# Performance work log

Measured on AMD Instinct MI355X. Metric: run time of the kernel, lower is better.

The kernel has to match this reference:

```python
import jax, jax.numpy as jnp
import numpy as np

N_SEQ, L, DH, DX, M, G, N_TOK, N_MEM, N_TYP = 1024, 64, 256, 128, 8192, 4096, 10000, 262144, 64

def setup_inputs() -> dict:
    key = jax.random.key(0)
    ks = jax.random.split(key, 16)
    s_q = 1.0 / np.sqrt(2 * DH)
    s_k = 1.0 / np.sqrt(DH)
    s_r = 1.0 / np.sqrt(2 * DH + DX)
    msk = jax.random.randint(ks[4], (N_SEQ, L), 0, 2).astype(jnp.int32)
    msk = msk.at[:, 0].set(1)  # guarantee >=1 valid position per sequence
    return {
        "mem": jax.random.randint(ks[0], (N_MEM,), 0, N_TOK),
        "grp": jax.random.randint(ks[1], (N_MEM,), 0, G),
        "pos2grp": jax.random.randint(ks[2], (N_SEQ, L), 0, G),
        "h_grp": jax.random.normal(ks[3], (N_SEQ, L, DH), jnp.float32),
        "msk": msk,
        "idx": jnp.sort(jax.random.randint(ks[5], (M,), 0, N_SEQ)),
        "src": jax.random.randint(ks[6], (M,), 0, L),
        "dst": jax.random.randint(ks[7], (M,), 0, L),
        "typ": jax.random.randint(ks[8], (M, N_TYP), 0, 2).astype(jnp.int32),
        "tok_emb": jax.random.normal(ks[9], (N_TOK, DX), jnp.float32),
        "Wq": jax.random.normal(ks[10], (2 * DH, DH), jnp.float32) * s_q,
        "bq": jnp.zeros((DH,), jnp.float32),
        "Wk": jax.random.normal(ks[11], (DH, DH), jnp.float32) * s_k,
        "bk": jnp.zeros((DH,), jnp.float32),
        "Wrel": jax.random.normal(ks[12], (2 * DH + DX, N_TYP), jnp.float32) * s_r,
        "brel": jnp.zeros((N_TYP,), jnp.float32),
    }

def reference(mem, grp, pos2grp, h_grp, msk, idx, src, dst, typ,
              tok_emb, Wq, bq, Wk, bk, Wrel, brel):
    # z_grp = scatter_sum(tok_encoder(mem), grp, 0)[pos2grp]  -> (n, l, dx)
    z = jax.ops.segment_sum(tok_emb[mem], grp, num_segments=G)
    z_grp = z[pos2grp]
    # q = cat(h_grp[idx, src], h_grp[idx, dst])  -> (M, 2*dh)
    q = jnp.concatenate([h_grp[idx, src], h_grp[idx, dst]], axis=-1)
    qp = q @ Wq + bq                                    # (M, dh)
    kp = jnp.einsum('nld,de->nle', h_grp, Wk) + bk      # (n, l, dh)
    # repeat_interleave(nq) over sorted-by-group queries == gather by idx
    scores = jnp.einsum('mld,md->ml', kp[idx], qp) / jnp.sqrt(jnp.float32(DH))
    scores = jnp.where(msk[idx].astype(bool), scores, -jnp.inf)
    attn = jax.nn.softmax(scores, axis=1)               # (M, l)
    ctx = jnp.einsum('ml,mlv->mv', attn, z_grp[idx])    # (M, dx)
    logit = jnp.concatenate([q, ctx], axis=-1) @ Wrel + brel  # (M, n_typ)
    return logit
```

## Files before the change

### kernel.cpp

```cpp
#include <hip/hip_runtime.h>
#include <math.h>

#define N_SEQ 1024
#define LL 64
#define DH 256
#define DX 128
#define MQ 8192
#define GG 4096
#define NTYP 64
#define NMEM 262144

typedef __attribute__((ext_vector_type(8))) short short8v;
typedef __attribute__((ext_vector_type(4))) float float4v;

__device__ __forceinline__ unsigned short f2bf(float x) {
    unsigned int u = __float_as_uint(x);
    u += 0x7FFFu + ((u >> 16) & 1u);
    return (unsigned short)(u >> 16);
}

__global__ __launch_bounds__(256) void k_init(const float* __restrict__ Wq,
                                              unsigned short* __restrict__ WqB,
                                              int4* __restrict__ cnt4,
                                              const int* __restrict__ idx,
                                              int* __restrict__ ofs_n) {
    int b = blockIdx.x, tid = threadIdx.x;
    if (b < 128) {
        int i = (b * 256 + tid) * 4;
        float4 v = *(const float4*)(Wq + i);
        ushort4 o;
        o.x = f2bf(v.x); o.y = f2bf(v.y); o.z = f2bf(v.z); o.w = f2bf(v.w);
        *(ushort4*)(WqB + i) = o;
    } else if (b < 132) {
        cnt4[(b - 128) * 256 + tid] = (int4){0, 0, 0, 0};
    } else {
        int n = (b - 132) * 256 + tid;
        int lo = 0, hi = MQ;
        while (lo < hi) {
            int mid = (lo + hi) >> 1;
            if (idx[mid] < n) lo = mid + 1; else hi = mid;
        }
        ofs_n[n] = lo;
        if (n == 0) ofs_n[N_SEQ] = MQ;
    }
}

__global__ __launch_bounds__(256) void k_histw(const int* __restrict__ grp,
                                               int* __restrict__ cnt,
                                               int* __restrict__ rank,
                                               const float* __restrict__ Wk,
                                               const float* __restrict__ bq,
                                               const unsigned short* __restrict__ WqB,
                                               const float* __restrict__ Wrel,
                                               const float* __restrict__ brel,
                                               unsigned short* __restrict__ BT,
                                               float* __restrict__ bias) {
    __shared__ __align__(16) unsigned short A[16 * 256];
    __shared__ float bred[16][17];
    int b = blockIdx.x, tid = threadIdx.x;
    if (b < 1024) {
        int i = b * 256 + tid;
        rank[i] = atomicAdd(&cnt[grp[i]], 1);
        return;
    }
    int b2 = b - 1024;
    if (b2 < 16) {
        int n0 = b2 * 16;
        {
            int r = tid >> 4;
            int kc = (tid & 15) * 16;
            const float4* s4 = (const float4*)(Wk + (size_t)(n0 + r) * 256 + kc);
            unsigned short* Arow = A + r * 256;
#pragma unroll
            for (int j = 0; j < 2; ++j) {
                float4 lo = s4[j * 2], hi = s4[j * 2 + 1];
                unsigned short tmp[8];
                tmp[0] = f2bf(lo.x); tmp[1] = f2bf(lo.y);
                tmp[2] = f2bf(lo.z); tmp[3] = f2bf(lo.w);
                tmp[4] = f2bf(hi.x); tmp[5] = f2bf(hi.y);
                tmp[6] = f2bf(hi.z); tmp[7] = f2bf(hi.w);
                int c = (kc >> 3) + j;
                int cs = (c & ~7) | ((c & 7) ^ (r & 7));
                *(int4*)(Arow + cs * 8) = *(int4*)tmp;
            }
        }
        __syncthreads();
        int w = tid >> 6, lane = tid & 63;
        int r = lane & 15, kq = lane >> 4;
        float4v acc[8];
#pragma unroll
        for (int t = 0; t < 8; ++t) acc[t] = (float4v){0.f, 0.f, 0.f, 0.f};
        const unsigned short* Arow = A + r * 256;
#pragma unroll
        for (int ks = 0; ks < 8; ++ks) {
            int c = ks * 4 + kq;
            int cs = (c & ~7) | ((c & 7) ^ (r & 7));
            short8v a = *(const short8v*)(Arow + cs * 8);
            int kk = ks * 32 + kq * 8;
#pragma unroll
            for (int t = 0; t < 8; ++t) {
                int jcol = w * 128 + t * 16 + r;
                short8v bf = *(const short8v*)(WqB + (size_t)jcol * 256 + kk);
                acc[t] = __builtin_amdgcn_mfma_f32_16x16x32_bf16(a, bf, acc[t], 0, 0, 0);
            }
        }
#pragma unroll
        for (int t = 0; t < 8; ++t) {
            int jcol = w * 128 + t * 16 + r;
#pragma unroll
            for (int j = 0; j < 4; ++j)
                BT[(size_t)(n0 + kq * 4 + j) * 512 + jcol] = f2bf(acc[t][j]);
        }
        {
            int n16 = tid >> 4, seg = tid & 15;
            const float* wkr = Wk + (size_t)(n0 + n16) * 256 + seg * 16;
            const float* bqr = bq + seg * 16;
            float pb = 0.f;
#pragma unroll
            for (int i = 0; i < 16; ++i) pb += wkr[i] * bqr[i];
            bred[n16][seg] = pb;
        }
        __syncthreads();
        if (tid < 16) {
            float s = 0.f;
#pragma unroll
            for (int k2 = 0; k2 < 16; ++k2) s += bred[tid][k2];
            bias[n0 + tid] = s;
        }
    } else {
        int t0 = (b2 - 16) * 16;
#pragma unroll
        for (int jj = 0; jj < 2; ++jj) {
            int j = tid + jj * 256;
            const float* wr = Wrel + (size_t)j * NTYP + t0;
#pragma unroll
            for (int tt = 0; tt < 16; ++tt)
                BT[(size_t)(256 + t0 + tt) * 512 + j] = f2bf(wr[tt]);
        }
        if (b2 == 16 && tid < 64) bias[256 + tid] = brel[tid];
    }
}

__global__ __launch_bounds__(256) void k_sg(const int* __restrict__ cnt,
                                            int* __restrict__ ofs,
                                            const float* __restrict__ h_grp,
                                            const int* __restrict__ idx,
                                            const int* __restrict__ srcv,
                                            const int* __restrict__ dstv,
                                            const unsigned short* __restrict__ BT,
                                            const float* __restrict__ bias,
                                            unsigned short* __restrict__ qkb,
                                            float* __restrict__ part) {
    __shared__ __align__(16) unsigned short A[16 * 512];
    __shared__ int ns[16], ss[16], dsv[16];
    int b = blockIdx.x, tid = threadIdx.x;
    if (b == 0) {
        int* wsum = (int*)A;
        int lane = tid & 63, w = tid >> 6;
        int c[16];
        int tsum = 0;
        int base0 = tid * 16;
#pragma unroll
        for (int j = 0; j < 16; ++j) { c[j] = cnt[base0 + j]; tsum += c[j]; }
        int v = tsum;
        for (int o2 = 1; o2 < 64; o2 <<= 1) {
            int t = __shfl_up(v, o2);
            if (lane >= o2) v += t;
        }
        if (lane == 63) wsum[w] = v;
        __syncthreads();
        int wb = 0;
#pragma unroll
        for (int q2 = 0; q2 < 4; ++q2) if (q2 < w) wb += wsum[q2];
        int base = wb + v - tsum;
#pragma unroll
        for (int j = 0; j < 16; ++j) { ofs[base0 + j] = base; base += c[j]; }
        return;
    }
    int bid = b - 1;
    int swz = (bid & 7) * 64 + (bid >> 3);
    int m0 = swz * 16;
    if (tid < 16) {
        int m = m0 + tid;
        ns[tid] = idx[m];
        ss[tid] = srcv[m];
        dsv[tid] = dstv[m];
    }
    __syncthreads();
    {
        int r = tid >> 4;
        int kc = (tid & 15) * 32;
        const float* src = h_grp +
            ((size_t)ns[r] * LL + (kc < 256 ? ss[r] : dsv[r])) * DH + (kc & 255);
        const float4* s4 = (const float4*)src;
        float4 f[8];
#pragma unroll
        for (int j = 0; j < 8; ++j) f[j] = s4[j];
        unsigned short* Arow = A + r * 512;
#pragma unroll
        for (int j = 0; j < 4; ++j) {
            int c = (kc >> 3) + j;
            int cs = (c & ~7) | ((c & 7) ^ (r & 7));
            unsigned short tmp[8];
            float4 lo = f[j * 2], hi = f[j * 2 + 1];
            tmp[0] = f2bf(lo.x); tmp[1] = f2bf(lo.y);
            tmp[2] = f2bf(lo.z); tmp[3] = f2bf(lo.w);
            tmp[4] = f2bf(hi.x); tmp[5] = f2bf(hi.y);
            tmp[6] = f2bf(hi.z); tmp[7] = f2bf(hi.w);
            *(int4*)(Arow + cs * 8) = *(int4*)tmp;
        }
    }
    __syncthreads();

    int w = tid >> 6, lane = tid & 63;
    int r = lane & 15;
    int q = lane >> 4;
    int n0 = w * 80;
    float4v acc[5];
#pragma unroll
    for (int t = 0; t < 5; ++t) {
        float b3 = bias[n0 + t * 16 + r];
        acc[t] = (float4v){b3, b3, b3, b3};
    }
    const unsigned short* Arow = A + r * 512;
#pragma unroll 2
    for (int ks = 0; ks < 16; ++ks) {
        int c = ks * 4 + q;
        int cs = (c & ~7) | ((c & 7) ^ (r & 7));
        short8v a = *(const short8v*)(Arow + cs * 8);
        int kk = ks * 32 + q * 8;
#pragma unroll
        for (int t = 0; t < 5; ++t) {
            int n = n0 + t * 16 + r;
            short8v b3 = *(const short8v*)(BT + (size_t)n * 512 + kk);
            acc[t] = __builtin_amdgcn_mfma_f32_16x16x32_bf16(a, b3, acc[t], 0, 0, 0);
        }
    }
#pragma unroll
    for (int t = 0; t < 5; ++t) {
        int n = n0 + t * 16 + r;
        if (n < 256) {
#pragma unroll
            for (int j = 0; j < 4; ++j)
                qkb[(size_t)(m0 + q * 4 + j) * 256 + n] = f2bf(acc[t][j]);
        } else {
#pragma unroll
            for (int j = 0; j < 4; ++j)
                part[(size_t)(m0 + q * 4 + j) * NTYP + (n - 256)] = acc[t][j];
        }
    }
}

__global__ __launch_bounds__(256) void k_permute(const int* __restrict__ grp,
                                                 const int* __restrict__ mem,
                                                 const int* __restrict__ ofs,
                                                 const int* __restrict__ rank,
                                                 int* __restrict__ tok_sorted) {
    int i = blockIdx.x * 256 + threadIdx.x;
    if (i < NMEM) tok_sorted[ofs[grp[i]] + rank[i]] = mem[i];
}

__global__ __launch_bounds__(128) void k_zsum(const int* __restrict__ ofs,
                                              const int* __restrict__ cnt,
                                              const int* __restrict__ tok_sorted,
                                              const float* __restrict__ tok_emb,
                                              const float* __restrict__ Wrel,
                                              float* __restrict__ zw) {
    __shared__ int idxs[128];
    __shared__ float red[4][128];
    __shared__ float zs[128];
    int g = blockIdx.x;
    int tid = threadIdx.x;
    int gq = tid >> 5;
    int s = tid & 31;
    int start = ofs[g], n = cnt[g];
    float4 a0 = {0.f, 0.f, 0.f, 0.f}, a1 = {0.f, 0.f, 0.f, 0.f};
    for (int j0 = 0; j0 < n; j0 += 128) {
        __syncthreads();
        int rem = n - j0;
        if (tid < rem) idxs[tid] = tok_sorted[start + j0 + tid];
        __syncthreads();
        int kmax = rem < 128 ? rem : 128;
        int k = gq;
        for (; k + 4 < kmax; k += 8) {
            const float4* r0 = (const float4*)(tok_emb + (size_t)idxs[k] * DX);
            const float4* r1 = (const float4*)(tok_emb + (size_t)idxs[k + 4] * DX);
            float4 v0 = r0[s], v1 = r1[s];
            a0.x += v0.x; a0.y += v0.y; a0.z += v0.z; a0.w += v0.w;
            a1.x += v1.x; a1.y += v1.y; a1.z += v1.z; a1.w += v1.w;
        }
        if (k < kmax) {
            const float4* r0 = (const float4*)(tok_emb + (size_t)idxs[k] * DX);
            float4 v0 = r0[s];
            a0.x += v0.x; a0.y += v0.y; a0.z += v0.z; a0.w += v0.w;
        }
    }
    a0.x += a1.x; a0.y += a1.y; a0.z += a1.z; a0.w += a1.w;
    ((float4*)red[gq])[s] = a0;
    __syncthreads();
    zs[tid] = red[0][tid] + red[1][tid] + red[2][tid] + red[3][tid];
    __syncthreads();
    if (tid < NTYP) {
        float a2s = 0.f;
#pragma unroll 8
        for (int v = 0; v < DX; ++v)
            a2s += zs[v] * Wrel[(size_t)(512 + v) * NTYP + tid];
        zw[(size_t)g * NTYP + tid] = a2s;
    }
}

__global__ __launch_bounds__(256) void k_attn9(const float* __restrict__ h_grp,
                                               const int* __restrict__ ofs_n,
                                               const int* __restrict__ pos2grp,
                                               const int* __restrict__ msk,
                                               const float* __restrict__ zw,
                                               const unsigned short* __restrict__ qkb,
                                               const float* __restrict__ part,
                                               float* __restrict__ out) {
    __shared__ __align__(16) unsigned short zwT[64][72];
    __shared__ __align__(16) unsigned short PsT[16][72];
    __shared__ float red0[4][16], red1[4][16];

    int bid = blockIdx.x;
    int n = (bid & 7) * 128 + (bid >> 3);
    int start = ofs_n[n];
    int nq = ofs_n[n + 1] - start;
    if (nq <= 0) return;

    int tid = threadIdx.x;
    int w = tid >> 6, lane = tid & 63;
    int q15 = lane & 15, kq = lane >> 4;

    int mk = msk[n * LL + lane];
    int gv = pos2grp[n * LL + lane];

    {
        int l = 16 * w + (lane >> 2);
        int cb = (lane & 3) * 16;
        int gl = __shfl(gv, l);
        const float4* zr4 = (const float4*)(zw + (size_t)gl * NTYP + cb);
#pragma unroll
        for (int i4 = 0; i4 < 4; ++i4) {
            float4 zv = zr4[i4];
            zwT[cb + i4 * 4 + 0][l] = f2bf(zv.x);
            zwT[cb + i4 * 4 + 1][l] = f2bf(zv.y);
            zwT[cb + i4 * 4 + 2][l] = f2bf(zv.z);
            zwT[cb + i4 * 4 + 3][l] = f2bf(zv.w);
        }
    }

    const float* hrow = h_grp + ((size_t)n * LL + 16 * w + q15) * DH;
    short8v afrag[8];
#pragma unroll
    for (int ks = 0; ks < 8; ++ks) {
        const float4* p = (const float4*)(hrow + ks * 32 + kq * 8);
        float4 f0 = p[0], f1 = p[1];
        unsigned short t[8];
        t[0] = f2bf(f0.x); t[1] = f2bf(f0.y);
        t[2] = f2bf(f0.z); t[3] = f2bf(f0.w);
        t[4] = f2bf(f1.x); t[5] = f2bf(f1.y);
        t[6] = f2bf(f1.z); t[7] = f2bf(f1.w);
        afrag[ks] = *(short8v*)t;
    }
    __syncthreads();

    for (int t0 = 0; t0 < nq; t0 += 16) {
        int nqt = nq - t0; if (nqt > 16) nqt = 16;
        if (t0 > 0) __syncthreads();

        int mq = start + t0 + (q15 < nqt ? q15 : 0);
        const unsigned short* qrow = qkb + (size_t)mq * 256;
        float4v sacc = (float4v){0.f, 0.f, 0.f, 0.f};
#pragma unroll
        for (int ks = 0; ks < 8; ++ks) {
            short8v b = *(const short8v*)(qrow + ks * 32 + kq * 8);
            sacc = __builtin_amdgcn_mfma_f32_16x16x32_bf16(afrag[ks], b, sacc, 0, 0, 0);
        }
        float sv[4];
#pragma unroll
        for (int j = 0; j < 4; ++j) {
            int l = 16 * w + kq * 4 + j;
            int mkl = __shfl(mk, l);
            sv[j] = mkl ? sacc[j] * 0.0625f : -INFINITY;
        }
        float pmax = fmaxf(fmaxf(sv[0], sv[1]), fmaxf(sv[2], sv[3]));
        pmax = fmaxf(pmax, __shfl_xor(pmax, 16));
        pmax = fmaxf(pmax, __shfl_xor(pmax, 32));
        if (lane < 16) red0[w][lane] = pmax;
        __syncthreads();
        float mx = fmaxf(fmaxf(red0[0][q15], red0[1][q15]),
                         fmaxf(red0[2][q15], red0[3][q15]));
        float pe[4];
        float psum = 0.f;
#pragma unroll
        for (int j = 0; j < 4; ++j) { pe[j] = __expf(sv[j] - mx); psum += pe[j]; }
        psum += __shfl_xor(psum, 16);
        psum += __shfl_xor(psum, 32);
        if (lane < 16) red1[w][lane] = psum;
        __syncthreads();
        float inv = 1.0f / (red1[0][q15] + red1[1][q15] + red1[2][q15] + red1[3][q15]);
        ushort4 pk;
        pk.x = f2bf(pe[0] * inv); pk.y = f2bf(pe[1] * inv);
        pk.z = f2bf(pe[2] * inv); pk.w = f2bf(pe[3] * inv);
        *(ushort4*)(&PsT[q15][16 * w + kq * 4]) = pk;
        __syncthreads();

        float4v cacc[4];
#pragma unroll
        for (int ct = 0; ct < 4; ++ct) cacc[ct] = (float4v){0.f, 0.f, 0.f, 0.f};
#pragma unroll
        for (int ks = 0; ks < 2; ++ks) {
            short8v a = *(const short8v*)(&PsT[q15][ks * 32 + kq * 8]);
#pragma unroll
            for (int ct = 0; ct < 4; ++ct) {
                short8v b = *(const short8v*)(&zwT[ct * 16 + q15][ks * 32 + kq * 8]);
                cacc[ct] = __builtin_amdgcn_mfma_f32_16x16x32_bf16(a, b, cacc[ct], 0, 0, 0);
            }
        }
#pragma unroll
        for (int ct = 0; ct < 4; ++ct) {
            int col = ct * 16 + q15;
#pragma unroll
            for (int j = 0; j < 4; ++j) {
                int qrow2 = kq * 4 + j;
                if (qrow2 < nqt) {
                    size_t m = (size_t)(start + t0 + qrow2);
                    out[m * NTYP + col] = part[m * NTYP + col] + cacc[ct][j];
                }
            }
        }
    }
}

extern "C" void kernel_launch(void* const* d_in, const int* in_sizes, int n_in,
                              void* d_out, int out_size, void* d_ws, size_t ws_size,
                              hipStream_t stream) {
    const int*   mem     = (const int*)d_in[0];
    const int*   grp     = (const int*)d_in[1];
    const int*   pos2grp = (const int*)d_in[2];
    const float* h_grp   = (const float*)d_in[3];
    const int*   msk     = (const int*)d_in[4];
    const int*   idx     = (const int*)d_in[5];
    const int*   srcv    = (const int*)d_in[6];
    const int*   dstv    = (const int*)d_in[7];
    const float* tok_emb = (const float*)d_in[9];
    const float* Wq      = (const float*)d_in[10];
    const float* bq      = (const float*)d_in[11];
    const float* Wk      = (const float*)d_in[12];
    const float* bk      = (const float*)d_in[13];
    const float* Wrel    = (const float*)d_in[14];
    const float* brel    = (const float*)d_in[15];
    float* out = (float*)d_out;
    (void)bk;

    float* ws = (float*)d_ws;
    size_t off = 0;
    float* zw   = ws + off; off += (size_t)GG * NTYP;
    unsigned short* qkb = (unsigned short*)(ws + off); off += (size_t)MQ * 256 / 2;
    float* part = ws + off; off += (size_t)MQ * NTYP;
    float* bias = ws + off; off += 320;
    unsigned short* BT  = (unsigned short*)(ws + off); off += (320 * 512) / 2;
    unsigned short* WqB = (unsigned short*)(ws + off); off += (512 * 256) / 2;
    int* cnt        = (int*)(ws + off); off += GG;
    int* ofs        = (int*)(ws + off); off += GG;
    int* rank       = (int*)(ws + off); off += NMEM;
    int* tok_sorted = (int*)(ws + off); off += NMEM;
    int* ofs_n      = (int*)(ws + off); off += N_SEQ + 1;

    k_init<<<136, 256, 0, stream>>>(Wq, WqB, (int4*)cnt, idx, ofs_n);

    k_histw<<<1044, 256, 0, stream>>>(grp, cnt, rank, Wk, bq, WqB, Wrel, brel,
                                      BT, bias);

    k_sg<<<513, 256, 0, stream>>>(cnt, ofs, h_grp, idx, srcv, dstv, BT, bias,
                                  qkb, part);

    k_permute<<<NMEM / 256, 256, 0, stream>>>(grp, mem, ofs, rank, tok_sorted);

    k_zsum<<<GG, 128, 0, stream>>>(ofs, cnt, tok_sorted, tok_emb, Wrel, zw);

    k_attn9<<<N_SEQ, 256, 0, stream>>>(h_grp, ofs_n, pos2grp, msk, zw, qkb, part, out);
}
```

Before: 102.1 us.

## Move score/softmax into permute kernel, leaving light ctx kernel after zsum

Splits the attention kernel in two. The score MFMA and masked softmax now run in extra blocks of the permute launch, before zsum, and the bf16 probabilities are written to a global Pg buffer. The final kernel only builds zwT and does the P×zw MFMA plus the add of the partial logits. This moves the h_grp load and score work off the tail of the dependency chain and overlaps it with the scatter permute, at the cost of an extra global round trip for the probabilities.

New measurement: 104.4 us. 1.02x slower.

```diff
diff --git a/kernel.cpp b/kernel.cpp
--- a/kernel.cpp
+++ b/kernel.cpp
@@ -251,13 +251,86 @@
     }
 }
 
-__global__ __launch_bounds__(256) void k_permute(const int* __restrict__ grp,
-                                                 const int* __restrict__ mem,
-                                                 const int* __restrict__ ofs,
-                                                 const int* __restrict__ rank,
-                                                 int* __restrict__ tok_sorted) {
-    int i = blockIdx.x * 256 + threadIdx.x;
-    if (i < NMEM) tok_sorted[ofs[grp[i]] + rank[i]] = mem[i];
+__global__ __launch_bounds__(256) void k_pscore(const int* __restrict__ grp,
+                                                const int* __restrict__ mem,
+                                                const int* __restrict__ ofs,
+                                                const int* __restrict__ rank,
+                                                int* __restrict__ tok_sorted,
+                                                const float* __restrict__ h_grp,
+                                                const int* __restrict__ ofs_n,
+                                                const int* __restrict__ msk,
+                                                const unsigned short* __restrict__ qkb,
+                                                unsigned short* __restrict__ Pg) {
+    __shared__ float red0[4][16], red1[4][16];
+    int b = blockIdx.x, tid = threadIdx.x;
+    if (b < 1024) {
+        int i = b * 256 + tid;
+        tok_sorted[ofs[grp[i]] + rank[i]] = mem[i];
+        return;
+    }
+    int bid = b - 1024;
+    int n = (bid & 7) * 128 + (bid >> 3);
+    int start = ofs_n[n];
+    int nq = ofs_n[n + 1] - start;
+    if (nq <= 0) return;
+
+    int w = tid >> 6, lane = tid & 63;
+    int q15 = lane & 15, kq = lane >> 4;
+    int mk = msk[n * LL + lane];
+
+    const float* hrow = h_grp + ((size_t)n * LL + 16 * w + q15) * DH;
+    short8v afrag[8];
+#pragma unroll
+    for (int ks = 0; ks < 8; ++ks) {
+        const float4* p = (const float4*)(hrow + ks * 32 + kq * 8);
+        float4 f0 = p[0], f1 = p[1];
+        unsigned short t[8];
+        t[0] = f2bf(f0.x); t[1] = f2bf(f0.y);
+        t[2] = f2bf(f0.z); t[3] = f2bf(f0.w);
+        t[4] = f2bf(f1.x); t[5] = f2bf(f1.y);
+        t[6] = f2bf(f1.z); t[7] = f2bf(f1.w);
+        afrag[ks] = *(short8v*)t;
+    }
+
+    for (int t0 = 0; t0 < nq; t0 += 16) {
+        int nqt = nq - t0; if (nqt > 16) nqt = 16;
+        int mq = start + t0 + (q15 < nqt ? q15 : 0);
+        const unsigned short* qrow = qkb + (size_t)mq * 256;
+        float4v sacc = (float4v){0.f, 0.f, 0.f, 0.f};
+#pragma unroll
+        for (int ks = 0; ks < 8; ++ks) {
+            short8v b3 = *(const short8v*)(qrow + ks * 32 + kq * 8);
+            sacc = __builtin_amdgcn_mfma_f32_16x16x32_bf16(afrag[ks], b3, sacc, 0, 0, 0);
+        }
+        float sv[4];
+#pragma unroll
+        for (int j = 0; j < 4; ++j) {
+            int l = 16 * w + kq * 4 + j;
+            int mkl = __shfl(mk, l);
+            sv[j] = mkl ? sacc[j] * 0.0625f : -INFINITY;
+        }
+        float pmax = fmaxf(fmaxf(sv[0], sv[1]), fmaxf(sv[2], sv[3]));
+        pmax = fmaxf(pmax, __shfl_xor(pmax, 16));
+        pmax = fmaxf(pmax, __shfl_xor(pmax, 32));
+        if (lane < 16) red0[w][lane] = pmax;
+        __syncthreads();
+        float mx = fmaxf(fmaxf(red0[0][q15], red0[1][q15]),
+                         fmaxf(red0[2][q15], red0[3][q15]));
+        float pe[4];
+        float psum = 0.f;
+#pragma unroll
+        for (int j = 0; j < 4; ++j) { pe[j] = __expf(sv[j] - mx); psum += pe[j]; }
+        psum += __shfl_xor(psum, 16);
+        psum += __shfl_xor(psum, 32);
+        if (lane < 16) red1[w][lane] = psum;
+        __syncthreads();
+        float inv = 1.0f / (red1[0][q15] + red1[1][q15] + red1[2][q15] + red1[3][q15]);
+        ushort4 pk;
+        pk.x = f2bf(pe[0] * inv); pk.y = f2bf(pe[1] * inv);
+        pk.z = f2bf(pe[2] * inv); pk.w = f2bf(pe[3] * inv);
+        if (q15 < nqt)
+            *(ushort4*)(Pg + (size_t)(start + t0 + q15) * NTYP + 16 * w + kq * 4) = pk;
+    }
 }
 
 __global__ __launch_bounds__(128) void k_zsum(const int* __restrict__ ofs,
@@ -309,18 +382,13 @@
     }
 }
 
-__global__ __launch_bounds__(256) void k_attn9(const float* __restrict__ h_grp,
-                                               const int* __restrict__ ofs_n,
-                                               const int* __restrict__ pos2grp,
-                                               const int* __restrict__ msk,
-                                               const float* __restrict__ zw,
-                                               const unsigned short* __restrict__ qkb,
-                                               const float* __restrict__ part,
-                                               float* __restrict__ out) {
+__global__ __launch_bounds__(256) void k_ctx(const int* __restrict__ ofs_n,
+                                             const int* __restrict__ pos2grp,
+                                             const float* __restrict__ zw,
+                                             const unsigned short* __restrict__ Pg,
+                                             const float* __restrict__ part,
+                                             float* __restrict__ out) {
     __shared__ __align__(16) unsigned short zwT[64][72];
-    __shared__ __align__(16) unsigned short PsT[16][72];
-    __shared__ float red0[4][16], red1[4][16];
-
     int bid = blockIdx.x;
     int n = (bid & 7) * 128 + (bid >> 3);
     int start = ofs_n[n];
@@ -331,7 +399,6 @@
     int w = tid >> 6, lane = tid & 63;
     int q15 = lane & 15, kq = lane >> 4;
 
-    int mk = msk[n * LL + lane];
     int gv = pos2grp[n * LL + lane];
 
     {
@@ -348,69 +415,17 @@
             zwT[cb + i4 * 4 + 3][l] = f2bf(zv.w);
         }
     }
-
-    const float* hrow = h_grp + ((size_t)n * LL + 16 * w + q15) * DH;
-    short8v afrag[8];
-#pragma unroll
-    for (int ks = 0; ks < 8; ++ks) {
-        const float4* p = (const float4*)(hrow + ks * 32 + kq * 8);
-        float4 f0 = p[0], f1 = p[1];
-        unsigned short t[8];
-        t[0] = f2bf(f0.x); t[1] = f2bf(f0.y);
-        t[2] = f2bf(f0.z); t[3] = f2bf(f0.w);
-        t[4] = f2bf(f1.x); t[5] = f2bf(f1.y);
-        t[6] = f2bf(f1.z); t[7] = f2bf(f1.w);
-        afrag[ks] = *(short8v*)t;
-    }
     __syncthreads();
 
     for (int t0 = 0; t0 < nq; t0 += 16) {
         int nqt = nq - t0; if (nqt > 16) nqt = 16;
-        if (t0 > 0) __syncthreads();
-
         int mq = start + t0 + (q15 < nqt ? q15 : 0);
-        const unsigned short* qrow = qkb + (size_t)mq * 256;
-        float4v sacc = (float4v){0.f, 0.f, 0.f, 0.f};
-#pragma unroll
-        for (int ks = 0; ks < 8; ++ks) {
-            short8v b = *(const short8v*)(qrow + ks * 32 + kq * 8);
-            sacc = __builtin_amdgcn_mfma_f32_16x16x32_bf16(afrag[ks], b, sacc, 0, 0, 0);
-        }
-        float sv[4];
-#pragma unroll
-        for (int j = 0; j < 4; ++j) {
-            int l = 16 * w + kq * 4 + j;
-            int mkl = __shfl(mk, l);
-            sv[j] = mkl ? sacc[j] * 0.0625f : -INFINITY;
-        }
-        float pmax = fmaxf(fmaxf(sv[0], sv[1]), fmaxf(sv[2], sv[3]));
-        pmax = fmaxf(pmax, __shfl_xor(pmax, 16));
-        pmax = fmaxf(pmax, __shfl_xor(pmax, 32));
-        if (lane < 16) red0[w][lane] = pmax;
-        __syncthreads();
-        float mx = fmaxf(fmaxf(red0[0][q15], red0[1][q15]),
-                         fmaxf(red0[2][q15], red0[3][q15]));
-        float pe[4];
-        float psum = 0.f;
-#pragma unroll
-        for (int j = 0; j < 4; ++j) { pe[j] = __expf(sv[j] - mx); psum += pe[j]; }
-        psum += __shfl_xor(psum, 16);
-        psum += __shfl_xor(psum, 32);
-        if (lane < 16) red1[w][lane] = psum;
-        __syncthreads();
-        float inv = 1.0f / (red1[0][q15] + red1[1][q15] + red1[2][q15] + red1[3][q15]);
-        ushort4 pk;
-        pk.x = f2bf(pe[0] * inv); pk.y = f2bf(pe[1] * inv);
-        pk.z = f2bf(pe[2] * inv); pk.w = f2bf(pe[3] * inv);
-        *(ushort4*)(&PsT[q15][16 * w + kq * 4]) = pk;
-        __syncthreads();
-
         float4v cacc[4];
 #pragma unroll
         for (int ct = 0; ct < 4; ++ct) cacc[ct] = (float4v){0.f, 0.f, 0.f, 0.f};
 #pragma unroll
         for (int ks = 0; ks < 2; ++ks) {
-            short8v a = *(const short8v*)(&PsT[q15][ks * 32 + kq * 8]);
+            short8v a = *(const short8v*)(Pg + (size_t)mq * NTYP + ks * 32 + kq * 8);
 #pragma unroll
             for (int ct = 0; ct < 4; ++ct) {
                 short8v b = *(const short8v*)(&zwT[ct * 16 + q15][ks * 32 + kq * 8]);
@@ -458,6 +473,7 @@
     float* zw   = ws + off; off += (size_t)GG * NTYP;
     unsigned short* qkb = (unsigned short*)(ws + off); off += (size_t)MQ * 256 / 2;
     float* part = ws + off; off += (size_t)MQ * NTYP;
+    unsigned short* Pg  = (unsigned short*)(ws + off); off += (size_t)MQ * NTYP / 2;
     float* bias = ws + off; off += 320;
     unsigned short* BT  = (unsigned short*)(ws + off); off += (320 * 512) / 2;
     unsigned short* WqB = (unsigned short*)(ws + off); off += (512 * 256) / 2;
@@ -475,9 +491,10 @@
     k_sg<<<513, 256, 0, stream>>>(cnt, ofs, h_grp, idx, srcv, dstv, BT, bias,
                                   qkb, part);
 
-    k_permute<<<NMEM / 256, 256, 0, stream>>>(grp, mem, ofs, rank, tok_sorted);
+    k_pscore<<<2048, 256, 0, stream>>>(grp, mem, ofs, rank, tok_sorted,
+                                       h_grp, ofs_n, msk, qkb, Pg);
 
     k_zsum<<<GG, 128, 0, stream>>>(ofs, cnt, tok_sorted, tok_emb, Wrel, zw);
 
-    k_attn9<<<N_SEQ, 256, 0, stream>>>(h_grp, ofs_n, pos2grp, msk, zw, qkb, part, out);
-}
+    k_ctx<<<N_SEQ, 256, 0, stream>>>(ofs_n, pos2grp, zw, Pg, part, out);
+}
```
